# Performance work log

Hardware: AMD Instinct MI355X
Metric: run time of the kernel (lower is better)

The kernel has to match this reference:

```python
import jax, jax.numpy as jnp
import numpy as np

N_NODES = 50000
N_EDGES = 800000
IN_FEATS = 32
OUT_FEATS = 32
NUM_HEADS = 4


def setup_inputs() -> dict:
    key = jax.random.key(0)
    ks = jax.random.split(key, 12)
    H, F, IN = NUM_HEADS, OUT_FEATS, IN_FEATS
    h = jax.random.normal(ks[0], (N_NODES, IN), dtype=jnp.float32)
    src = jax.random.randint(ks[1], (N_EDGES,), 0, N_NODES, dtype=jnp.int64)
    dst = jax.random.randint(ks[2], (N_EDGES,), 0, N_NODES, dtype=jnp.int64)
    s = 0.1
    W_gat = jax.random.normal(ks[3], (IN, H * F), dtype=jnp.float32) * s
    attn_l = jax.random.normal(ks[4], (H, F), dtype=jnp.float32) * s
    attn_r = jax.random.normal(ks[5], (H, F), dtype=jnp.float32) * s
    W_ih = jax.random.normal(ks[6], (3 * F, H * F), dtype=jnp.float32) * s
    W_hh = jax.random.normal(ks[7], (3 * F, F), dtype=jnp.float32) * s
    b_ih = jax.random.normal(ks[8], (3 * F,), dtype=jnp.float32) * s
    b_hh = jax.random.normal(ks[9], (3 * F,), dtype=jnp.float32) * s
    return {"h": h, "W_gat": W_gat, "attn_l": attn_l, "attn_r": attn_r,
            "W_ih": W_ih, "W_hh": W_hh, "b_ih": b_ih, "b_hh": b_hh,
            "src": src, "dst": dst}


def reference(h, W_gat, attn_l, attn_r, W_ih, W_hh, b_ih, b_hh, src, dst):
    N = h.shape[0]
    H, F = attn_l.shape
    # --- GATConv ---
    feat = (h @ W_gat).reshape(N, H, F)                      # (N,H,F)
    el = jnp.einsum('nhf,hf->nh', feat, attn_l)              # (N,H)
    er = jnp.einsum('nhf,hf->nh', feat, attn_r)              # (N,H)
    e = jax.nn.leaky_relu(el[src] + er[dst], 0.2)            # (E,H) edge logits
    emax = jax.ops.segment_max(e, dst, num_segments=N)       # per-dst max (stable)
    ee = jnp.exp(e - emax[dst])
    denom = jax.ops.segment_sum(ee, dst, num_segments=N)
    alpha = ee / denom[dst]                                  # segment softmax (E,H)
    msg = feat[src] * alpha[:, :, None]                      # (E,H,F)
    agg = jax.ops.segment_sum(msg, dst, num_segments=N)      # (N,H,F)
    x = agg.reshape(N, H * F)
    # --- GRUCell (torch semantics, gate order r,z,n) ---
    gi = x @ W_ih.T + b_ih                                   # (N,3F)
    gh = h @ W_hh.T + b_hh                                   # (N,3F)
    i_r, i_z, i_n = jnp.split(gi, 3, axis=1)
    h_r, h_z, h_n = jnp.split(gh, 3, axis=1)
    r = jax.nn.sigmoid(i_r + h_r)
    z = jax.nn.sigmoid(i_z + h_z)
    n = jnp.tanh(i_n + r * h_n)
    h_new = (1.0 - z) * n + z * h
    return jax.nn.elu(h_new)
```

## Files before the change

### kernel.cpp

```cpp
#include <hip/hip_runtime.h>
#include <hip/hip_bf16.h>
#include <cmath>

#define N_NODES 50000
#define N_EDGES 800000
#define CAP 64

#define NBINS 196
#define BIN_CAP 8192

#define WCB_ITEMS (144 * 32)
#define WCB_BLOCKS (WCB_ITEMS / 256)
#define WC_ITEMS (192 * 160)
#define WC_BLOCKS (WC_ITEMS / 256)

#define P1_EPT 8
#define P1_EPB (256 * P1_EPT)
#define P1_BLOCKS ((N_EDGES + P1_EPB - 1) / P1_EPB)
#define FEAT_BLOCKS ((N_NODES / 16 + 3) / 4)

typedef __attribute__((ext_vector_type(8))) short bf16x8;
typedef __attribute__((ext_vector_type(4))) float f32x4;

__device__ inline short bfbits(float x) {
    __hip_bfloat16 t = __float2bfloat16(x);
    return *reinterpret_cast<short*>(&t);
}

__device__ inline unsigned char f32_to_fp8(float x) {
    return (unsigned char)(__builtin_amdgcn_cvt_pk_fp8_f32(x, x, 0, false) & 0xff);
}

__global__ __launch_bounds__(256) void k_prep0(
        const float* __restrict__ Wg, const float* __restrict__ al,
        const float* __restrict__ ar, const float* __restrict__ Wih,
        const float* __restrict__ Whh, __hip_bfloat16* __restrict__ Wcomb,
        __hip_bfloat16* __restrict__ Wc, int* __restrict__ bin_cursor) {
    const int t = threadIdx.x;
    if (blockIdx.x < WCB_BLOCKS) {
        const int idx = blockIdx.x * 256 + t;
        const int row = idx >> 5, k = idx & 31;
        float v = 0.f;
        if (row < 128) {
            v = Wg[k * 128 + row];
        } else if (row < 136) {
            const int hd = (row - 128) & 3;
            const float* a = (row < 132) ? (al + hd * 32) : (ar + hd * 32);
            const float* w = Wg + k * 128 + hd * 32;
#pragma unroll
            for (int f = 0; f < 32; ++f) v = fmaf(w[f], a[f], v);
        }
        Wcomb[idx] = __float2bfloat16(v);
        return;
    }
    if (blockIdx.x < WCB_BLOCKS + WC_BLOCKS) {
        const int idx = (blockIdx.x - WCB_BLOCKS) * 256 + t;
        const int r = idx / 160, k = idx - r * 160;
        float v = 0.f;
        if (r < 96) { if (k < 128) v = Wih[r * 128 + k]; }
        else        { if (k >= 128) v = Whh[(r - 96) * 32 + (k - 128)]; }
        Wc[idx] = __float2bfloat16(v);
        return;
    }
    if (t < NBINS) bin_cursor[t] = 0;
}

__global__ __launch_bounds__(256) void k_part_feat(
        const float* __restrict__ h, const __hip_bfloat16* __restrict__ Wcomb,
        const int* __restrict__ src, const int* __restrict__ dst,
        int* __restrict__ bin_cursor, unsigned* __restrict__ bin_buf,
        unsigned char* __restrict__ feat, float* __restrict__ el,
        float* __restrict__ er) {
    const int t = threadIdx.x;
    if (blockIdx.x < P1_BLOCKS) {
        __shared__ int bcnt[256], bofs[256], cur[256], gbase[256];
        __shared__ int wt4[4];
        __shared__ unsigned stage[P1_EPB];
        bcnt[t] = 0;
        __syncthreads();
        int bn[P1_EPT];
        unsigned pk[P1_EPT];
        const int ebase = blockIdx.x * P1_EPB + t;
#pragma unroll
        for (int q = 0; q < P1_EPT; ++q) {
            const int e = ebase + q * 256;
            if (e < N_EDGES) {
                const int d = dst[e];
                bn[q] = d >> 8;
                pk[q] = (unsigned)src[e] | ((unsigned)(d & 255) << 16);
                atomicAdd(&bcnt[bn[q]], 1);
            } else bn[q] = -1;
        }
        __syncthreads();
        {
            const int wave = t >> 6, lane = t & 63;
            const int vv = bcnt[t];
            int x = vv;
#pragma unroll
            for (int m = 1; m < 64; m <<= 1) {
                const int y = __shfl_up(x, m, 64);
                if (lane >= m) x += y;
            }
            if (lane == 63) wt4[wave] = x;
            __syncthreads();
            int wb = 0;
#pragma unroll
            for (int i = 0; i < 4; ++i) if (i < wave) wb += wt4[i];
            const int off = wb + x - vv;
            bofs[t] = off;
            cur[t] = off;
            gbase[t] = (vv > 0) ? atomicAdd(&bin_cursor[t], vv) : 0;
        }
        __syncthreads();
#pragma unroll
        for (int q = 0; q < P1_EPT; ++q)
            if (bn[q] >= 0) stage[atomicAdd(&cur[bn[q]], 1)] = pk[q];
        __syncthreads();
        if (t < NBINS) {
            const int c = bcnt[t], o = bofs[t], g = gbase[t];
            unsigned* bb = bin_buf + (size_t)t * BIN_CAP;
            for (int j = 0; j < c; ++j) {
                const int gi = g + j;
                if (gi < BIN_CAP) bb[gi] = stage[o + j];
            }
        }
        return;
    }
    __shared__ unsigned char sbuf8[4][16][136];
    const int lane = t & 63, wave = t >> 6;
    const int li = lane & 15, quad = lane >> 4;
    const int mt = (blockIdx.x - P1_BLOCKS) * 4 + wave;
    if (mt >= N_NODES / 16) return;
    const int m_base = mt * 16;
    bf16x8 a;
    {
        const float4* hp = (const float4*)(h + (size_t)(m_base + li) * 32 + quad * 8);
        const float4 f0 = hp[0], f1 = hp[1];
        a[0] = bfbits(f0.x); a[1] = bfbits(f0.y); a[2] = bfbits(f0.z); a[3] = bfbits(f0.w);
        a[4] = bfbits(f1.x); a[5] = bfbits(f1.y); a[6] = bfbits(f1.z); a[7] = bfbits(f1.w);
    }
    f32x4 acc[9];
#pragma unroll
    for (int j = 0; j < 9; ++j) acc[j] = (f32x4){0.f, 0.f, 0.f, 0.f};
#pragma unroll
    for (int j = 0; j < 9; ++j) {
        const bf16x8 b = *(const bf16x8*)(Wcomb + (size_t)(j * 16 + li) * 32 + quad * 8);
        acc[j] = __builtin_amdgcn_mfma_f32_16x16x32_bf16(a, b, acc[j], 0, 0, 0);
    }
#pragma unroll
    for (int j = 0; j < 8; ++j)
#pragma unroll
        for (int i = 0; i < 4; ++i)
            sbuf8[wave][quad * 4 + i][j * 16 + li] = f32_to_fp8(acc[j][i]);
    __builtin_amdgcn_wave_barrier();
#pragma unroll
    for (int rep = 0; rep < 4; ++rep) {
        const int row = rep * 4 + quad;
        const unsigned long long v = *(const unsigned long long*)(&sbuf8[wave][row][li * 8]);
        *(unsigned long long*)(feat + (size_t)(m_base + row) * 128 + li * 8) = v;
    }
    if (li < 8) {
#pragma unroll
        for (int i = 0; i < 4; ++i) {
            const int m = m_base + quad * 4 + i;
            if (li < 4) el[m * 4 + li] = acc[8][i];
            else        er[m * 4 + (li - 4)] = acc[8][i];
        }
    }
}

__global__ __launch_bounds__(256) void k_scat2(
        const int* __restrict__ bin_cursor, const unsigned* __restrict__ bin_buf,
        int* __restrict__ srcs_p, int* __restrict__ counts) {
    __shared__ int lcnt[256];
    const int t = threadIdx.x;
    const int b = blockIdx.x;
    lcnt[t] = 0;
    __syncthreads();
    const int cb = min(bin_cursor[b], BIN_CAP);
    const unsigned* bb = bin_buf + (size_t)b * BIN_CAP;
    for (int i = t; i < cb; i += 256) {
        const unsigned p = bb[i];
        const int dl = p >> 16;
        const int s = p & 0xffff;
        const int pos = atomicAdd(&lcnt[dl], 1);
        if (pos < CAP) srcs_p[(size_t)(b * 256 + dl) * CAP + pos] = s;
    }
    __syncthreads();
    const int node = b * 256 + t;
    if (node < N_NODES) counts[node] = lcnt[t];
}

__global__ __launch_bounds__(256) void k_aggr_gru(
        const int* __restrict__ counts, const int* __restrict__ srcs_p,
        const unsigned char* __restrict__ feat,
        const float* __restrict__ el, const float* __restrict__ er,
        const float* __restrict__ h, const __hip_bfloat16* __restrict__ Wc,
        const float* __restrict__ bih, const float* __restrict__ bhh,
        float* __restrict__ out) {
    __shared__ __hip_bfloat16 xh_tile[16][160];
    __shared__ int   sl_s[4][64];
    __shared__ float eel_s[4][256];
    __shared__ float ex[2][3][16][16];
    const int wave = threadIdx.x >> 6;
    const int lane = threadIdx.x & 63;
    int*   sl  = sl_s[wave];
    float* eel = eel_s[wave];
    const int hs = lane & 3;
    const int hc = lane >> 4;
    const int mbase = blockIdx.x * 16;

    for (int u = 0; u < 4; ++u) {
        const int row = wave * 4 + u;
        const int n = mbase + row;
        const float ern = er[n * 4 + hs];
        const int cnt = min(counts[n], CAP);
        float ax = 0.f, ay = 0.f, psum = 0.f;
        if (lane < cnt) sl[lane] = srcs_p[(size_t)n * CAP + lane];
        __builtin_amdgcn_wave_barrier();
#pragma unroll
        for (int p = 0; p < 4; ++p) {
            const int j = p * 64 + lane;
            if (j < cnt * 4) {
                const int s = sl[j >> 2];
                float v = el[s * 4 + hs] + ern;
                v = v > 0.f ? v : 0.2f * v;
                const float e = expf(v);
                eel[j] = e;
                psum += e;
            }
        }
        __builtin_amdgcn_wave_barrier();
        int i = 0;
        for (; i + 4 <= cnt; i += 4) {
            const int s0 = sl[i], s1 = sl[i + 1], s2 = sl[i + 2], s3 = sl[i + 3];
            const int u0 = ((const unsigned short*)(feat + (size_t)s0 * 128))[lane];
            const int u1 = ((const unsigned short*)(feat + (size_t)s1 * 128))[lane];
            const int u2 = ((const unsigned short*)(feat + (size_t)s2 * 128))[lane];
            const int u3 = ((const unsigned short*)(feat + (size_t)s3 * 128))[lane];
            const float w0 = eel[i * 4 + hc];
            const float w1 = eel[(i + 1) * 4 + hc];
            const float w2 = eel[(i + 2) * 4 + hc];
            const float w3 = eel[(i + 3) * 4 + hc];
            ax = fmaf(w0, __builtin_amdgcn_cvt_f32_fp8(u0, 0), ax);
            ay = fmaf(w0, __builtin_amdgcn_cvt_f32_fp8(u0, 1), ay);
            ax = fmaf(w1, __builtin_amdgcn_cvt_f32_fp8(u1, 0), ax);
            ay = fmaf(w1, __builtin_amdgcn_cvt_f32_fp8(u1, 1), ay);
            ax = fmaf(w2, __builtin_amdgcn_cvt_f32_fp8(u2, 0), ax);
            ay = fmaf(w2, __builtin_amdgcn_cvt_f32_fp8(u2, 1), ay);
            ax = fmaf(w3, __builtin_amdgcn_cvt_f32_fp8(u3, 0), ax);
            ay = fmaf(w3, __builtin_amdgcn_cvt_f32_fp8(u3, 1), ay);
        }
        for (; i < cnt; ++i) {
            const int u0 = ((const unsigned short*)(feat + (size_t)sl[i] * 128))[lane];
            const float w = eel[i * 4 + hc];
            ax = fmaf(w, __builtin_amdgcn_cvt_f32_fp8(u0, 0), ax);
            ay = fmaf(w, __builtin_amdgcn_cvt_f32_fp8(u0, 1), ay);
        }
        __builtin_amdgcn_wave_barrier();
#pragma unroll
        for (int m = 4; m < 64; m <<= 1) psum += __shfl_xor(psum, m, 64);
        const float dn = __shfl(psum, hc, 64);
        const float inv = (cnt > 0) ? 1.f / dn : 0.f;
        __hip_bfloat162 v2;
        v2.x = __float2bfloat16(ax * inv);
        v2.y = __float2bfloat16(ay * inv);
        ((__hip_bfloat162*)&xh_tile[row][0])[lane] = v2;
        if (lane < 32) xh_tile[row][128 + lane] = __float2bfloat16(h[(size_t)n * 32 + lane]);
    }
    __syncthreads();

    const int li = lane & 15, quad = lane >> 4;
    const int cb = wave >> 1;
    const int ghrole = wave & 1;
    bf16x8 a[5];
#pragma unroll
    for (int s = 0; s < 5; ++s)
        a[s] = *(const bf16x8*)((const char*)&xh_tile[0][0] + li * 320 + s * 64 + quad * 16);
    f32x4 acc[3];
#pragma unroll
    for (int g = 0; g < 3; ++g) {
        acc[g] = (f32x4){0.f, 0.f, 0.f, 0.f};
        const int j = g * 2 + cb + ghrole * 6;
        const bf16x8* bp = (const bf16x8*)(Wc + (size_t)(j * 16 + li) * 160 + quad * 8);
        acc[g] = __builtin_amdgcn_mfma_f32_16x16x32_bf16(a[0], bp[0],  acc[g], 0, 0, 0);
        acc[g] = __builtin_amdgcn_mfma_f32_16x16x32_bf16(a[1], bp[4],  acc[g], 0, 0, 0);
        acc[g] = __builtin_amdgcn_mfma_f32_16x16x32_bf16(a[2], bp[8],  acc[g], 0, 0, 0);
        acc[g] = __builtin_amdgcn_mfma_f32_16x16x32_bf16(a[3], bp[12], acc[g], 0, 0, 0);
        acc[g] = __builtin_amdgcn_mfma_f32_16x16x32_bf16(a[4], bp[16], acc[g], 0, 0, 0);
    }
    if (ghrole) {
#pragma unroll
        for (int g = 0; g < 3; ++g)
#pragma unroll
            for (int i = 0; i < 4; ++i)
                ex[cb][g][quad * 4 + i][li] = acc[g][i];
    }
    __syncthreads();
    if (!ghrole) {
        const int c = cb * 16 + li;
        const float bir = bih[c],      bhr = bhh[c];
        const float biz = bih[32 + c], bhz = bhh[32 + c];
        const float bin = bih[64 + c], bhn = bhh[64 + c];
#pragma unroll
        for (int i = 0; i < 4; ++i) {
            const int row = quad * 4 + i;
            const int m = mbase + row;
            const float gr = acc[0][i] + bir + ex[cb][0][row][li] + bhr;
            const float gz = acc[1][i] + biz + ex[cb][1][row][li] + bhz;
            const float r = 1.f / (1.f + expf(-gr));
            const float z = 1.f / (1.f + expf(-gz));
            const float nn = tanhf(acc[2][i] + bin + r * (ex[cb][2][row][li] + bhn));
            const float hv = h[(size_t)m * 32 + c];
            const float hn = (1.f - z) * nn + z * hv;
            out[(size_t)m * 32 + c] = hn > 0.f ? hn : expm1f(hn);
        }
    }
}

extern "C" void kernel_launch(void* const* d_in, const int* in_sizes, int n_in,
                              void* d_out, int out_size, void* d_ws, size_t ws_size,
                              hipStream_t stream) {
    const float* h   = (const float*)d_in[0];
    const float* Wg  = (const float*)d_in[1];
    const float* al  = (const float*)d_in[2];
    const float* ar  = (const float*)d_in[3];
    const float* Wih = (const float*)d_in[4];
    const float* Whh = (const float*)d_in[5];
    const float* bih = (const float*)d_in[6];
    const float* bhh = (const float*)d_in[7];
    const int* src   = (const int*)d_in[8];
    const int* dst   = (const int*)d_in[9];
    float* out = (float*)d_out;

    float* el = (float*)d_ws;
    float* er = el + (size_t)N_NODES * 4;
    unsigned char* feat8 = (unsigned char*)(er + (size_t)N_NODES * 4);
    __hip_bfloat16* Wc    = (__hip_bfloat16*)(feat8 + (size_t)N_NODES * 128);
    __hip_bfloat16* Wcomb = Wc + 192 * 160;
    int* counts  = (int*)(Wcomb + WCB_ITEMS);
    int* srcs_p  = counts + N_NODES;
    int* bin_cursor = srcs_p + (size_t)N_NODES * CAP;
    unsigned* bin_buf = (unsigned*)(bin_cursor + NBINS);

    k_prep0<<<WCB_BLOCKS + WC_BLOCKS + 1, 256, 0, stream>>>(
        Wg, al, ar, Wih, Whh, Wcomb, Wc, bin_cursor);
    k_part_feat<<<P1_BLOCKS + FEAT_BLOCKS, 256, 0, stream>>>(
        h, Wcomb, src, dst, bin_cursor, bin_buf, feat8, el, er);
    k_scat2<<<NBINS, 256, 0, stream>>>(bin_cursor, bin_buf, srcs_p, counts);
    k_aggr_gru<<<N_NODES / 16, 256, 0, stream>>>(
        counts, srcs_p, feat8, el, er, h, Wc, bih, bhh, out);
}
```

Baseline: 155.4 us.

## Vectorize edge loads, pad bin cursors, widen aggregation gathers to 4 bytes

Several changes land together. The partition pass now loads src/dst with int4 vector loads, and each thread takes a contiguous block of edges. Per-bin global cursors are padded by 32 ints so their atomics do not share cache lines. The scatter pass reads the bin buffer as uint4. The aggregation kernel preloads the source lists for all four rows up front, and each half-wave gathers a different edge with 4-byte fp8 loads. The two halves are combined with a cross-lane shuffle. This cuts the number of narrow gather instructions, at the cost of more shared memory and an extra reduction step.

```diff
diff --git a/kernel.cpp b/kernel.cpp
--- a/kernel.cpp
+++ b/kernel.cpp
@@ -8,6 +8,7 @@
 
 #define NBINS 196
 #define BIN_CAP 8192
+#define CUR_PAD 32
 
 #define WCB_ITEMS (144 * 32)
 #define WCB_BLOCKS (WCB_ITEMS / 256)
@@ -62,7 +63,7 @@
         Wc[idx] = __float2bfloat16(v);
         return;
     }
-    if (t < NBINS) bin_cursor[t] = 0;
+    if (t < NBINS) bin_cursor[t * CUR_PAD] = 0;
 }
 
 __global__ __launch_bounds__(256) void k_part_feat(
@@ -80,16 +81,22 @@
         __syncthreads();
         int bn[P1_EPT];
         unsigned pk[P1_EPT];
-        const int ebase = blockIdx.x * P1_EPB + t;
-#pragma unroll
-        for (int q = 0; q < P1_EPT; ++q) {
-            const int e = ebase + q * 256;
-            if (e < N_EDGES) {
-                const int d = dst[e];
-                bn[q] = d >> 8;
-                pk[q] = (unsigned)src[e] | ((unsigned)(d & 255) << 16);
+        const int ebase = blockIdx.x * P1_EPB + t * P1_EPT;
+        if (ebase < N_EDGES) {
+            int dd[P1_EPT], ss[P1_EPT];
+            *(int4*)(dd)     = *(const int4*)(dst + ebase);
+            *(int4*)(dd + 4) = *(const int4*)(dst + ebase + 4);
+            *(int4*)(ss)     = *(const int4*)(src + ebase);
+            *(int4*)(ss + 4) = *(const int4*)(src + ebase + 4);
+#pragma unroll
+            for (int q = 0; q < P1_EPT; ++q) {
+                bn[q] = dd[q] >> 8;
+                pk[q] = (unsigned)ss[q] | ((unsigned)(dd[q] & 255) << 16);
                 atomicAdd(&bcnt[bn[q]], 1);
-            } else bn[q] = -1;
+            }
+        } else {
+#pragma unroll
+            for (int q = 0; q < P1_EPT; ++q) bn[q] = -1;
         }
         __syncthreads();
         {
@@ -109,7 +116,7 @@
             const int off = wb + x - vv;
             bofs[t] = off;
             cur[t] = off;
-            gbase[t] = (vv > 0) ? atomicAdd(&bin_cursor[t], vv) : 0;
+            gbase[t] = (vv > 0) ? atomicAdd(&bin_cursor[t * CUR_PAD], vv) : 0;
         }
         __syncthreads();
 #pragma unroll
@@ -177,14 +184,20 @@
     const int b = blockIdx.x;
     lcnt[t] = 0;
     __syncthreads();
-    const int cb = min(bin_cursor[b], BIN_CAP);
-    const unsigned* bb = bin_buf + (size_t)b * BIN_CAP;
-    for (int i = t; i < cb; i += 256) {
-        const unsigned p = bb[i];
-        const int dl = p >> 16;
-        const int s = p & 0xffff;
-        const int pos = atomicAdd(&lcnt[dl], 1);
-        if (pos < CAP) srcs_p[(size_t)(b * 256 + dl) * CAP + pos] = s;
+    const int cb = min(bin_cursor[b * CUR_PAD], BIN_CAP);
+    const uint4* bb4 = (const uint4*)(bin_buf + (size_t)b * BIN_CAP);
+    for (int i = t * 4; i < cb; i += 1024) {
+        const uint4 p4 = bb4[i >> 2];
+#pragma unroll
+        for (int k = 0; k < 4; ++k) {
+            if (i + k < cb) {
+                const unsigned p = (&p4.x)[k];
+                const int dl = p >> 16;
+                const int s = p & 0xffff;
+                const int pos = atomicAdd(&lcnt[dl], 1);
+                if (pos < CAP) srcs_p[(size_t)(b * 256 + dl) * CAP + pos] = s;
+            }
+        }
     }
     __syncthreads();
     const int node = b * 256 + t;
@@ -199,25 +212,33 @@
         const float* __restrict__ bih, const float* __restrict__ bhh,
         float* __restrict__ out) {
     __shared__ __hip_bfloat16 xh_tile[16][160];
-    __shared__ int   sl_s[4][64];
+    __shared__ int   sl_s[4][4][64];
     __shared__ float eel_s[4][256];
     __shared__ float ex[2][3][16][16];
     const int wave = threadIdx.x >> 6;
     const int lane = threadIdx.x & 63;
-    int*   sl  = sl_s[wave];
     float* eel = eel_s[wave];
     const int hs = lane & 3;
-    const int hc = lane >> 4;
+    const int eh = lane >> 5;
+    const int fl = lane & 31;
+    const int hq = fl >> 3;
     const int mbase = blockIdx.x * 16;
 
+    int cnts[4];
+#pragma unroll
+    for (int u = 0; u < 4; ++u) {
+        const int n = mbase + wave * 4 + u;
+        cnts[u] = min(counts[n], CAP);
+        if (lane < cnts[u]) sl_s[wave][u][lane] = srcs_p[(size_t)n * CAP + lane];
+    }
+    __builtin_amdgcn_wave_barrier();
     for (int u = 0; u < 4; ++u) {
         const int row = wave * 4 + u;
         const int n = mbase + row;
         const float ern = er[n * 4 + hs];
-        const int cnt = min(counts[n], CAP);
-        float ax = 0.f, ay = 0.f, psum = 0.f;
-        if (lane < cnt) sl[lane] = srcs_p[(size_t)n * CAP + lane];
-        __builtin_amdgcn_wave_barrier();
+        const int cnt = cnts[u];
+        const int* sl = sl_s[wave][u];
+        float a0 = 0.f, a1 = 0.f, a2 = 0.f, a3 = 0.f, psum = 0.f;
 #pragma unroll
         for (int p = 0; p < 4; ++p) {
             const int j = p * 64 + lane;
@@ -232,41 +253,64 @@
         }
         __builtin_amdgcn_wave_barrier();
         int i = 0;
-        for (; i + 4 <= cnt; i += 4) {
-            const int s0 = sl[i], s1 = sl[i + 1], s2 = sl[i + 2], s3 = sl[i + 3];
-            const int u0 = ((const unsigned short*)(feat + (size_t)s0 * 128))[lane];
-            const int u1 = ((const unsigned short*)(feat + (size_t)s1 * 128))[lane];
-            const int u2 = ((const unsigned short*)(feat + (size_t)s2 * 128))[lane];
-            const int u3 = ((const unsigned short*)(feat + (size_t)s3 * 128))[lane];
-            const float w0 = eel[i * 4 + hc];
-            const float w1 = eel[(i + 1) * 4 + hc];
-            const float w2 = eel[(i + 2) * 4 + hc];
-            const float w3 = eel[(i + 3) * 4 + hc];
-            ax = fmaf(w0, __builtin_amdgcn_cvt_f32_fp8(u0, 0), ax);
-            ay = fmaf(w0, __builtin_amdgcn_cvt_f32_fp8(u0, 1), ay);
-            ax = fmaf(w1, __builtin_amdgcn_cvt_f32_fp8(u1, 0), ax);
-            ay = fmaf(w1, __builtin_amdgcn_cvt_f32_fp8(u1, 1), ay);
-            ax = fmaf(w2, __builtin_amdgcn_cvt_f32_fp8(u2, 0), ax);
-            ay = fmaf(w2, __builtin_amdgcn_cvt_f32_fp8(u2, 1), ay);
-            ax = fmaf(w3, __builtin_amdgcn_cvt_f32_fp8(u3, 0), ax);
-            ay = fmaf(w3, __builtin_amdgcn_cvt_f32_fp8(u3, 1), ay);
-        }
-        for (; i < cnt; ++i) {
-            const int u0 = ((const unsigned short*)(feat + (size_t)sl[i] * 128))[lane];
-            const float w = eel[i * 4 + hc];
-            ax = fmaf(w, __builtin_amdgcn_cvt_f32_fp8(u0, 0), ax);
-            ay = fmaf(w, __builtin_amdgcn_cvt_f32_fp8(u0, 1), ay);
+        for (; i + 8 <= cnt; i += 8) {
+            const int s0 = sl[i + eh],     s1 = sl[i + 2 + eh];
+            const int s2 = sl[i + 4 + eh], s3 = sl[i + 6 + eh];
+            const unsigned u0 = *(const unsigned*)(feat + (size_t)s0 * 128 + fl * 4);
+            const unsigned u1 = *(const unsigned*)(feat + (size_t)s1 * 128 + fl * 4);
+            const unsigned u2 = *(const unsigned*)(feat + (size_t)s2 * 128 + fl * 4);
+            const unsigned u3 = *(const unsigned*)(feat + (size_t)s3 * 128 + fl * 4);
+            const float w0 = eel[(i + eh) * 4 + hq];
+            const float w1 = eel[(i + 2 + eh) * 4 + hq];
+            const float w2 = eel[(i + 4 + eh) * 4 + hq];
+            const float w3 = eel[(i + 6 + eh) * 4 + hq];
+            a0 = fmaf(w0, __builtin_amdgcn_cvt_f32_fp8(u0, 0), a0);
+            a1 = fmaf(w0, __builtin_amdgcn_cvt_f32_fp8(u0, 1), a1);
+            a2 = fmaf(w0, __builtin_amdgcn_cvt_f32_fp8(u0, 2), a2);
+            a3 = fmaf(w0, __builtin_amdgcn_cvt_f32_fp8(u0, 3), a3);
+            a0 = fmaf(w1, __builtin_amdgcn_cvt_f32_fp8(u1, 0), a0);
+            a1 = fmaf(w1, __builtin_amdgcn_cvt_f32_fp8(u1, 1), a1);
+            a2 = fmaf(w1, __builtin_amdgcn_cvt_f32_fp8(u1, 2), a2);
+            a3 = fmaf(w1, __builtin_amdgcn_cvt_f32_fp8(u1, 3), a3);
+            a0 = fmaf(w2, __builtin_amdgcn_cvt_f32_fp8(u2, 0), a0);
+            a1 = fmaf(w2, __builtin_amdgcn_cvt_f32_fp8(u2, 1), a1);
+            a2 = fmaf(w2, __builtin_amdgcn_cvt_f32_fp8(u2, 2), a2);
+            a3 = fmaf(w2, __builtin_amdgcn_cvt_f32_fp8(u2, 3), a3);
+            a0 = fmaf(w3, __builtin_amdgcn_cvt_f32_fp8(u3, 0), a0);
+            a1 = fmaf(w3, __builtin_amdgcn_cvt_f32_fp8(u3, 1), a1);
+            a2 = fmaf(w3, __builtin_amdgcn_cvt_f32_fp8(u3, 2), a2);
+            a3 = fmaf(w3, __builtin_amdgcn_cvt_f32_fp8(u3, 3), a3);
+        }
+        for (; i < cnt; i += 2) {
+            const int e2 = i + eh;
+            if (e2 < cnt) {
+                const int s0 = sl[e2];
+                const unsigned u0 = *(const unsigned*)(feat + (size_t)s0 * 128 + fl * 4);
+                const float w0 = eel[e2 * 4 + hq];
+                a0 = fmaf(w0, __builtin_amdgcn_cvt_f32_fp8(u0, 0), a0);
+                a1 = fmaf(w0, __builtin_amdgcn_cvt_f32_fp8(u0, 1), a1);
+                a2 = fmaf(w0, __builtin_amdgcn_cvt_f32_fp8(u0, 2), a2);
+                a3 = fmaf(w0, __builtin_amdgcn_cvt_f32_fp8(u0, 3), a3);
+            }
         }
         __builtin_amdgcn_wave_barrier();
+        a0 += __shfl_xor(a0, 32, 64);
+        a1 += __shfl_xor(a1, 32, 64);
+        a2 += __shfl_xor(a2, 32, 64);
+        a3 += __shfl_xor(a3, 32, 64);
 #pragma unroll
         for (int m = 4; m < 64; m <<= 1) psum += __shfl_xor(psum, m, 64);
-        const float dn = __shfl(psum, hc, 64);
+        const float dn = __shfl(psum, hq, 64);
         const float inv = (cnt > 0) ? 1.f / dn : 0.f;
-        __hip_bfloat162 v2;
-        v2.x = __float2bfloat16(ax * inv);
-        v2.y = __float2bfloat16(ay * inv);
-        ((__hip_bfloat162*)&xh_tile[row][0])[lane] = v2;
-        if (lane < 32) xh_tile[row][128 + lane] = __float2bfloat16(h[(size_t)n * 32 + lane]);
+        if (lane < 32) {
+            __hip_bfloat162 p0, p1;
+            p0.x = __float2bfloat16(a0 * inv); p0.y = __float2bfloat16(a1 * inv);
+            p1.x = __float2bfloat16(a2 * inv); p1.y = __float2bfloat16(a3 * inv);
+            __hip_bfloat162* xp = (__hip_bfloat162*)&xh_tile[row][0];
+            xp[lane * 2]     = p0;
+            xp[lane * 2 + 1] = p1;
+            xh_tile[row][128 + lane] = __float2bfloat16(h[(size_t)n * 32 + lane]);
+        }
     }
     __syncthreads();
 
@@ -341,7 +385,7 @@
     int* counts  = (int*)(Wcomb + WCB_ITEMS);
     int* srcs_p  = counts + N_NODES;
     int* bin_cursor = srcs_p + (size_t)N_NODES * CAP;
-    unsigned* bin_buf = (unsigned*)(bin_cursor + NBINS);
+    unsigned* bin_buf = (unsigned*)(bin_cursor + NBINS * CUR_PAD);
 
     k_prep0<<<WCB_BLOCKS + WC_BLOCKS + 1, 256, 0, stream>>>(
         Wg, al, ar, Wih, Whh, Wcomb, Wc, bin_cursor);
```

Result: no change. 153.1 us (-1.5%).
